# Kernel optimization log

Measured on AMD Instinct MI355X. Metric: run time of the kernel, lower is better.

The kernel has to match this reference:

```python
import jax, jax.numpy as jnp
import numpy as np
from jax import lax

EPS = 1e-5
K_UP = 5
RATIO = 2
PAD = 2


def conv1x1(x, w):
    # x: (B,C,H,W), w: (O,C)
    return jnp.einsum('bchw,oc->bohw', x, w)


def bn(x, g, b, m, v):
    inv = g / jnp.sqrt(v + EPS)
    return x * inv[None, :, None, None] + (b - m * inv)[None, :, None, None]


def relu6(x):
    return jnp.clip(x, 0.0, 6.0)


def carafe_down(x, wc, bc, we, be):
    # content-aware reassembly kernels
    y = conv1x1(x, wc) + bc[None, :, None, None]              # (B, 64, H, W)
    y = lax.conv_general_dilated(
        y, we, window_strides=(RATIO, RATIO), padding=[(PAD, PAD), (PAD, PAD)],
        dimension_numbers=('NCHW', 'OIHW', 'NCHW')) + be[None, :, None, None]
    w = jax.nn.softmax(y, axis=1)                              # (B, 25, Ho, Wo)
    B, C, H, W = x.shape
    Ho, Wo = H // RATIO, W // RATIO
    xp = jnp.pad(x, ((0, 0), (0, 0), (PAD, PAD), (PAD, PAD)))
    out = jnp.zeros((B, C, Ho, Wo), x.dtype)
    k = 0
    for i in range(K_UP):
        for j in range(K_UP):
            patch = xp[:, :, i:i + RATIO * Ho:RATIO, j:j + RATIO * Wo:RATIO]
            out = out + patch * w[:, k][:, None]
            k += 1
    return out


def setup_inputs() -> dict:
    key = jax.random.key(0)
    ks = jax.random.split(key, 20)
    B, INP, H, W = 8, 64, 112, 112
    OUP, HID, CMID = 128, 384, 64

    def bn_params(k, c):
        k1, k2, k3, k4 = jax.random.split(k, 4)
        return (jax.random.uniform(k1, (c,), jnp.float32, 0.5, 1.5),
                jax.random.normal(k2, (c,), jnp.float32) * 0.1,
                jax.random.normal(k3, (c,), jnp.float32) * 0.1,
                jax.random.uniform(k4, (c,), jnp.float32, 0.5, 1.5))
    g1, b1, m1, v1 = bn_params(ks[1], HID)
    g2, b2, m2, v2 = bn_params(ks[2], HID)
    g3, b3, m3, v3 = bn_params(ks[3], OUP)
    return {
        'x': jax.random.normal(ks[0], (B, INP, H, W), jnp.float32),
        'w1': jax.random.normal(ks[4], (HID, INP), jnp.float32) / np.sqrt(INP),
        'g1': g1, 'b1': b1, 'm1': m1, 'v1': v1,
        'wc': jax.random.normal(ks[5], (CMID, HID), jnp.float32) / np.sqrt(HID),
        'bc': jax.random.normal(ks[6], (CMID,), jnp.float32) * 0.01,
        'we': jax.random.normal(ks[7], (K_UP**2, CMID, 5, 5), jnp.float32) / np.sqrt(CMID * 25),
        'be': jax.random.normal(ks[8], (K_UP**2,), jnp.float32) * 0.01,
        'g2': g2, 'b2': b2, 'm2': m2, 'v2': v2,
        'w2': jax.random.normal(ks[9], (OUP, HID), jnp.float32) / np.sqrt(HID),
        'g3': g3, 'b3': b3, 'm3': m3, 'v3': v3,
    }


def reference(x, w1, g1, b1, m1, v1, wc, bc, we, be, g2, b2, m2, v2, w2, g3, b3, m3, v3):
    # stride-2 InvertedResidualBlockCarafe (no identity): 1x1 expand -> BN -> ReLU6
    # -> CARAFE_downsample -> BN -> ReLU6 -> 1x1 project -> BN
    h = relu6(bn(conv1x1(x, w1), g1, b1, m1, v1))
    h = relu6(bn(carafe_down(h, wc, bc, we, be), g2, b2, m2, v2))
    return bn(conv1x1(h, w2), g3, b3, m3, v3)
```

## Files before the change

### kernel.cpp

```cpp
#include <hip/hip_runtime.h>
#include <hip/hip_bf16.h>
#include <type_traits>

#define EPS 1e-5f

typedef _Float16 half8 __attribute__((ext_vector_type(8)));
typedef _Float16 half4 __attribute__((ext_vector_type(4)));
typedef _Float16 half2v __attribute__((ext_vector_type(2)));
typedef float f32x4 __attribute__((ext_vector_type(4)));

__device__ __forceinline__ void gload_lds16(const void* gsrc, void* ldst) {
  __builtin_amdgcn_global_load_lds(
      (const __attribute__((address_space(1))) void*)gsrc,
      (__attribute__((address_space(3))) void*)ldst, 16, 0, 0);
}

__global__ __launch_bounds__(256) void fold_k(
    const float* __restrict__ w1, const float* __restrict__ g1, const float* __restrict__ b1,
    const float* __restrict__ m1, const float* __restrict__ v1,
    const float* __restrict__ wc,
    const float* __restrict__ g2, const float* __restrict__ b2,
    const float* __restrict__ m2, const float* __restrict__ v2,
    const float* __restrict__ w2, const float* __restrict__ g3, const float* __restrict__ b3,
    const float* __restrict__ m3, const float* __restrict__ v3,
    const float* __restrict__ we,
    _Float16* __restrict__ w1h, float* __restrict__ bias1,
    _Float16* __restrict__ wch,
    _Float16* __restrict__ w2h, float* __restrict__ bias3,
    float* __restrict__ s2, float* __restrict__ t2,
    _Float16* __restrict__ wa) {
  int i = blockIdx.x * 256 + threadIdx.x;
  if (i < 384 * 64) {
    int o = i >> 6;
    float inv = g1[o] / sqrtf(v1[o] + EPS);
    w1h[i] = (_Float16)(w1[i] * inv);
  }
  if (i < 64 * 384) wch[i] = (_Float16)wc[i];
  if (i < 128 * 384) {
    int o = i / 384;
    float inv = g3[o] / sqrtf(v3[o] + EPS);
    w2h[i] = (_Float16)(w2[i] * inv);
  }
  if (i < 384) {
    float inv = g1[i] / sqrtf(v1[i] + EPS);
    bias1[i] = b1[i] - m1[i] * inv;
    float inv2 = g2[i] / sqrtf(v2[i] + EPS);
    s2[i] = inv2;
    t2[i] = b2[i] - m2[i] * inv2;
  }
  if (i < 128) {
    float inv = g3[i] / sqrtf(v3[i] + EPS);
    bias3[i] = b3[i] - m3[i] * inv;
  }
  if (i < 51200) {
    int j = i & 7;
    int lane = (i >> 3) & 63;
    int f = i >> 9;
    int ocf = f & 1;
    int tap = (f >> 1) % 25;
    int ph = f / 50;
    int oc = ocf * 16 + (lane & 15);
    int cm = ph * 32 + (lane >> 4) * 8 + j;
    float v = (oc < 25) ? we[((size_t)oc * 64 + cm) * 25 + tap] : 0.f;
    wa[i] = (_Float16)v;
  }
}

template <int IC, int NPF, int ACT, int NOC, int NPXT, typename TI, typename TO>
__global__ __launch_bounds__(256) void gemm16_k(
    const TI* __restrict__ in, const _Float16* __restrict__ wh,
    const float* __restrict__ bias, TO* __restrict__ out, int npx) {
  constexpr int BPX = NPF * 64;
  constexpr int V = 16 / sizeof(TI);
  constexpr int CPR = BPX / V;
  constexpr int SPT = 32 * CPR / 256;
  constexpr int PAD = 16 / sizeof(TO);
  constexpr int CH = 16 / sizeof(TO);
  constexpr int SPAN = NPF * 16;
  constexpr int LPO = SPAN / CH;
  constexpr int OCPI = 64 / LPO;
  constexpr size_t XS_B = (size_t)32 * BPX * sizeof(TI);
  constexpr size_t OT_B = (size_t)64 * (BPX + PAD) * sizeof(TO);
  constexpr size_t SM_B = XS_B > OT_B ? XS_B : OT_B;
  using vec16 = std::conditional_t<std::is_same_v<TO, _Float16>, half8, float4>;

  __shared__ __align__(16) unsigned char smem[SM_B];
  TI (*xs)[BPX] = (TI (*)[BPX])smem;
  TO (*oT)[BPX + PAD] = (TO (*)[BPX + PAD])smem;

  const int tid = threadIdx.x;
  const int lane = tid & 63;
  const int w = tid >> 6;
  const int l15 = lane & 15;
  const int g = lane >> 4;
  const int wpx = w * SPAN;

  const int wg = blockIdx.x;
  const int xcd = wg & 7;
  const int s = wg >> 3;
  const int oct = s % NOC;
  const int gl = s / NOC;
  const int grp = gl * 8 + xcd;
  const int pxt = grp % NPXT;
  const int b = grp / NPXT;

  const int p0 = pxt * BPX;
  const int oc0 = oct * 64;
  const int OCT = NOC * 64;
  const TI* inb = in + (size_t)b * IC * npx + p0;

  f32x4 acc[4][NPF];
#pragma unroll
  for (int fo = 0; fo < 4; ++fo)
#pragma unroll
    for (int pf = 0; pf < NPF; ++pf)
      acc[fo][pf] = (f32x4){0.f, 0.f, 0.f, 0.f};

  for (int kk = 0; kk < IC; kk += 32) {
    __syncthreads();
    half8 a[4];
#pragma unroll
    for (int fo = 0; fo < 4; ++fo)
      a[fo] = *(const half8*)&wh[(size_t)(oc0 + fo * 16 + l15) * IC + kk + g * 8];
#pragma unroll
    for (int i = 0; i < SPT; ++i) {
      int sl = tid + 256 * i;
      int k = sl / CPR, q = sl - (sl / CPR) * CPR;
      int qg = q ^ (((k >> 3) & 1) << 2);
      gload_lds16(&inb[(size_t)(kk + k) * npx + qg * V],
                  (unsigned char*)smem + (size_t)sl * 16);
    }
    __syncthreads();
    half8 xb[NPF];
#pragma unroll
    for (int pf = 0; pf < NPF; ++pf) {
      const int px = wpx + pf * 16 + l15;
      const int q = px / V, e = px - (px / V) * V;
      const int col = (q ^ ((g & 1) << 2)) * V + e;
#pragma unroll
      for (int j = 0; j < 8; ++j)
        xb[pf][j] = (_Float16)xs[g * 8 + j][col];
    }
#pragma unroll
    for (int fo = 0; fo < 4; ++fo)
#pragma unroll
      for (int pf = 0; pf < NPF; ++pf)
        acc[fo][pf] = __builtin_amdgcn_mfma_f32_16x16x32_f16(
            a[fo], xb[pf], acc[fo][pf], 0, 0, 0);
  }
  __syncthreads();

#pragma unroll
  for (int fo = 0; fo < 4; ++fo) {
#pragma unroll
    for (int r = 0; r < 4; ++r) {
      float bz = bias[oc0 + fo * 16 + g * 4 + r];
#pragma unroll
      for (int pf = 0; pf < NPF; ++pf) {
        float v = acc[fo][pf][r] + bz;
        if (ACT) v = fminf(fmaxf(v, 0.f), 6.f);
        oT[fo * 16 + g * 4 + r][wpx + pf * 16 + l15] = (TO)v;
      }
    }
  }
#pragma unroll
  for (int i = 0; i < LPO; ++i) {
    int oc = i * OCPI + lane / LPO;
    int pxo = (lane % LPO) * CH;
    vec16 v = *(const vec16*)&oT[oc][wpx + pxo];
    *(vec16*)&out[((size_t)b * OCT + oc0 + oc) * npx + p0 + wpx + pxo] = v;
  }
}

__global__ __launch_bounds__(256) void mask_conv6_k(
    const _Float16* __restrict__ y, const _Float16* __restrict__ wa,
    const float* __restrict__ be, float* __restrict__ msk) {
  __shared__ _Float16 ysh[32][5][136];
  __shared__ float lsm[32][66];
  const int ho = blockIdx.x;
  const int b = blockIdx.y;
  const int tid = threadIdx.x;
  const int lane = tid & 63;
  const int w = tid >> 6;
  const int l15 = lane & 15;
  const int g = lane >> 4;
  const int wo = w * 16 + l15;
  const int woe = (wo < 56) ? wo : 55;
  const int ci0 = 2 * woe + 6;

  for (int i = tid; i < 640; i += 256) {
    int ch = i / 20; int rem = i - ch * 20; int ri = rem / 4; int q = rem & 3;
    *(uint*)&ysh[ch][ri][q * 2] = 0u;
  }
  for (int i = tid; i < 1280; i += 256) {
    int ch = i / 40; int rem = i - ch * 40; int ri = rem / 8; int q = rem & 7;
    *(uint*)&ysh[ch][ri][120 + q * 2] = 0u;
  }

  f32x4 acc[2] = {(f32x4){0.f, 0.f, 0.f, 0.f}, (f32x4){0.f, 0.f, 0.f, 0.f}};

  for (int ph = 0; ph < 2; ++ph) {
    __syncthreads();
    for (int i = tid; i < 2240; i += 256) {
      int ch = i / 70;
      int rem = i - ch * 70;
      int ri = rem / 14;
      int j8 = rem - ri * 14;
      int hi = 2 * ho - 2 + ri;
      half8 v = {0, 0, 0, 0, 0, 0, 0, 0};
      if ((unsigned)hi < 112u)
        v = *(const half8*)&y[((size_t)(b * 64 + ph * 32 + ch) * 112 + hi) * 112 + j8 * 8];
      *(half8*)&ysh[ch][ri][8 + j8 * 8] = v;
    }
    __syncthreads();

    const _Float16* wap = wa + (size_t)ph * 25600;
#pragma unroll
    for (int di = 0; di < 5; ++di) {
      half2v pa[8], pb[8];
      _Float16 pc[8];
#pragma unroll
      for (int j = 0; j < 8; ++j) {
        pa[j] = *(const half2v*)&ysh[g * 8 + j][di][ci0];
        pb[j] = *(const half2v*)&ysh[g * 8 + j][di][ci0 + 2];
        pc[j] = ysh[g * 8 + j][di][ci0 + 4];
      }
#pragma unroll
      for (int dj = 0; dj < 5; ++dj) {
        half8 bf;
#pragma unroll
        for (int j = 0; j < 8; ++j)
          bf[j] = (dj == 0) ? pa[j][0]
                : (dj == 1) ? pa[j][1]
                : (dj == 2) ? pb[j][0]
                : (dj == 3) ? pb[j][1]
                            : pc[j];
        const int tap = di * 5 + dj;
        half8 a0 = *(const half8*)&wap[(tap * 2 + 0) * 512 + lane * 8];
        half8 a1 = *(const half8*)&wap[(tap * 2 + 1) * 512 + lane * 8];
        acc[0] = __builtin_amdgcn_mfma_f32_16x16x32_f16(a0, bf, acc[0], 0, 0, 0);
        acc[1] = __builtin_amdgcn_mfma_f32_16x16x32_f16(a1, bf, acc[1], 0, 0, 0);
      }
    }
  }

#pragma unroll
  for (int ocf = 0; ocf < 2; ++ocf)
#pragma unroll
    for (int r = 0; r < 4; ++r)
      lsm[ocf * 16 + g * 4 + r][w * 16 + l15] = acc[ocf][r];
  __syncthreads();

  if (tid < 56) {
    float v[25];
    float mx = -1e30f;
#pragma unroll
    for (int k = 0; k < 25; ++k) {
      float s = lsm[k][tid] + be[k];
      v[k] = s;
      mx = fmaxf(mx, s);
    }
    float s = 0.f;
#pragma unroll
    for (int k = 0; k < 25; ++k) {
      v[k] = __expf(v[k] - mx);
      s += v[k];
    }
    float inv = 1.0f / s;
#pragma unroll
    for (int k = 0; k < 25; ++k)
      msk[((size_t)b * 25 + k) * 3136 + ho * 56 + tid] = v[k] * inv;
  }
}

__device__ __forceinline__ void stage_pair(float dst[2][19][120],
                                           const _Float16* __restrict__ hbase,
                                           int ho0, int tid) {
  for (int i = tid; i < 2 * 19 * 14; i += 512) {
    int ch = i / 266;
    int rem = i - ch * 266;
    int rr = rem / 14;
    int j8 = rem - rr * 14;
    int hi = 2 * ho0 - 2 + rr;
    float4 lo = {0.f, 0.f, 0.f, 0.f}, hi4 = {0.f, 0.f, 0.f, 0.f};
    if ((unsigned)hi < 112u) {
      half8 v = *(const half8*)&hbase[(size_t)ch * 12544 + hi * 112 + j8 * 8];
      lo = (float4){(float)v[0], (float)v[1], (float)v[2], (float)v[3]};
      hi4 = (float4){(float)v[4], (float)v[5], (float)v[6], (float)v[7]};
    }
    *(float4*)&dst[ch][rr][4 + j8 * 8] = lo;
    *(float4*)&dst[ch][rr][8 + j8 * 8] = hi4;
  }
}

__global__ __launch_bounds__(512) void carafe3_k(
    const _Float16* __restrict__ h, const float* __restrict__ msk,
    const float* __restrict__ s2, const float* __restrict__ t2,
    _Float16* __restrict__ h2) {
  __shared__ float ys[2][2][19][120];
  const int hx = blockIdx.x;
  const int b  = blockIdx.y;
  const int cz = blockIdx.z;
  const int ho0 = hx * 8;
  const int tid = threadIdx.x;
  const int r = tid / 56;
  const int c = tid - r * 56;
  const int c0 = cz * 24;

  for (int i = tid; i < 2 * 2 * 19 * 8; i += 512) {
    int bufi = i / 304;
    int rem = i - bufi * 304;
    int ch = rem / 152;
    int rem2 = rem - ch * 152;
    int rr = rem2 / 8;
    int p = rem2 - rr * 8;
    int col = (p < 4) ? p : (112 + p);
    ys[bufi][ch][rr][col] = 0.f;
  }

  float m[25];
  if (tid < 448) {
    const float* mp = msk + (size_t)b * 25 * 3136 + (ho0 + r) * 56 + c;
#pragma unroll
    for (int k = 0; k < 25; ++k) m[k] = mp[(size_t)k * 3136];
  }
  __syncthreads();

  stage_pair(ys[0], h + (size_t)(b * 384 + c0) * 12544, ho0, tid);
  __syncthreads();

#pragma unroll
  for (int p = 0; p < 12; ++p) {
    const int bf = p & 1;
    if (p + 1 < 12)
      stage_pair(ys[bf ^ 1], h + (size_t)(b * 384 + c0 + 2 * (p + 1)) * 12544,
                 ho0, tid);
    if (tid < 448) {
#pragma unroll
      for (int cl = 0; cl < 2; ++cl) {
        const int cc = c0 + 2 * p + cl;
        float acc = 0.f;
#pragma unroll
        for (int di = 0; di < 5; ++di) {
          const float* row = &ys[bf][cl][2 * r + di][2 * c + 2];
          float2 a01 = *(const float2*)&row[0];
          float2 a23 = *(const float2*)&row[2];
          float a4 = row[4];
          acc = fmaf(a01.x, m[di * 5 + 0], acc);
          acc = fmaf(a01.y, m[di * 5 + 1], acc);
          acc = fmaf(a23.x, m[di * 5 + 2], acc);
          acc = fmaf(a23.y, m[di * 5 + 3], acc);
          acc = fmaf(a4,    m[di * 5 + 4], acc);
        }
        float o = s2[cc] * acc + t2[cc];
        h2[((size_t)(b * 384 + cc) * 56 + ho0 + r) * 56 + c] =
            (_Float16)fminf(fmaxf(o, 0.f), 6.f);
      }
    }
    __syncthreads();
  }
}

extern "C" void kernel_launch(void* const* d_in, const int* in_sizes, int n_in,
                              void* d_out, int out_size, void* d_ws, size_t ws_size,
                              hipStream_t stream) {
  const float* x  = (const float*)d_in[0];
  const float* w1 = (const float*)d_in[1];
  const float* g1 = (const float*)d_in[2];
  const float* b1 = (const float*)d_in[3];
  const float* m1 = (const float*)d_in[4];
  const float* v1 = (const float*)d_in[5];
  const float* wc = (const float*)d_in[6];
  const float* bc = (const float*)d_in[7];
  const float* we = (const float*)d_in[8];
  const float* be = (const float*)d_in[9];
  const float* g2 = (const float*)d_in[10];
  const float* b2 = (const float*)d_in[11];
  const float* m2 = (const float*)d_in[12];
  const float* v2 = (const float*)d_in[13];
  const float* w2 = (const float*)d_in[14];
  const float* g3 = (const float*)d_in[15];
  const float* b3 = (const float*)d_in[16];
  const float* m3 = (const float*)d_in[17];
  const float* v3 = (const float*)d_in[18];
  float* out = (float*)d_out;

  _Float16* hq  = (_Float16*)d_ws;
  _Float16* yq  = hq + 38535168;
  _Float16* h2q = yq + 6422528;
  float* mskf   = (float*)(h2q + 9633792);
  float* bias1  = mskf + 627200;
  float* bias3  = bias1 + 384;
  float* s2     = bias3 + 128;
  float* t2     = s2 + 384;
  _Float16* w1h = (_Float16*)(t2 + 384);
  _Float16* wch = w1h + 24576;
  _Float16* w2h = wch + 24576;
  _Float16* wa  = w2h + 49152;

  fold_k<<<200, 256, 0, stream>>>(w1, g1, b1, m1, v1, wc, g2, b2, m2, v2,
                                  w2, g3, b3, m3, v3, we,
                                  w1h, bias1, wch, w2h, bias3, s2, t2, wa);

  gemm16_k<64, 2, 1, 6, 98, float, _Float16>
      <<<6 * 98 * 8, 256, 0, stream>>>(x, w1h, bias1, hq, 12544);

  gemm16_k<384, 2, 0, 1, 98, _Float16, _Float16>
      <<<1 * 98 * 8, 256, 0, stream>>>(hq, wch, bc, yq, 12544);

  mask_conv6_k<<<dim3(56, 8), 256, 0, stream>>>(yq, wa, be, mskf);

  carafe3_k<<<dim3(7, 8, 16), 512, 0, stream>>>(hq, mskf, s2, t2, h2q);

  gemm16_k<384, 1, 0, 2, 49, _Float16, float>
      <<<2 * 49 * 8, 256, 0, stream>>>(h2q, w2h, bias3, out, 3136);
}
```

Measured before the change: 146.6 us.

## Fuse expand 1x1 conv with content-encoder 1x1 conv in one kernel

Replaces the two separate GEMM launches (expand conv + BN/ReLU6, then the 384->64 content conv) with one kernel that computes each 64-pixel tile of the hidden activations in LDS and immediately feeds it into the second MFMA GEMM. It still writes the hidden activations to global memory for the CARAFE gather, but avoids re-reading them for the second GEMM and saves a launch. The trade-off is smaller tiles (64 pixels per block), extra barriers per hidden chunk, and weights reloaded from global per block.

New measurement: 185.3 us. +26.5%, slower.

```diff
diff --git a/kernel.cpp b/kernel.cpp
--- a/kernel.cpp
+++ b/kernel.cpp
@@ -63,6 +63,111 @@
     int cm = ph * 32 + (lane >> 4) * 8 + j;
     float v = (oc < 25) ? we[((size_t)oc * 64 + cm) * 25 + tap] : 0.f;
     wa[i] = (_Float16)v;
+  }
+}
+
+__global__ __launch_bounds__(256) void fused2_k(
+    const float* __restrict__ x, const _Float16* __restrict__ w1h,
+    const float* __restrict__ bias1, const _Float16* __restrict__ wch,
+    const float* __restrict__ bc, _Float16* __restrict__ hq,
+    _Float16* __restrict__ yq) {
+  __shared__ __align__(16) float xh[64][64];
+  __shared__ _Float16 hT[64][76];
+
+  const int tid = threadIdx.x;
+  const int lane = tid & 63;
+  const int w = tid >> 6;
+  const int l15 = lane & 15;
+  const int g = lane >> 4;
+  const int wpx = w * 16;
+  const int p0 = blockIdx.x * 64;
+  const int b = blockIdx.y;
+  const float* inb = x + (size_t)b * 64 * 12544 + p0;
+
+#pragma unroll
+  for (int i = 0; i < 4; ++i) {
+    int sl = tid + 256 * i;
+    int k = sl >> 4, q = sl & 15;
+    int qg = q ^ (((k >> 3) & 1) << 2);
+    gload_lds16(&inb[(size_t)k * 12544 + qg * 4],
+                (unsigned char*)xh + (size_t)sl * 16);
+  }
+  __syncthreads();
+
+  half8 xb[2];
+  {
+    const int px = wpx + l15;
+    const int q = px >> 2, e = px & 3;
+    const int col = (q ^ ((g & 1) << 2)) * 4 + e;
+#pragma unroll
+    for (int ks = 0; ks < 2; ++ks)
+#pragma unroll
+      for (int j = 0; j < 8; ++j)
+        xb[ks][j] = (_Float16)xh[ks * 32 + g * 8 + j][col];
+  }
+
+  f32x4 acc2[4];
+#pragma unroll
+  for (int fo2 = 0; fo2 < 4; ++fo2) acc2[fo2] = (f32x4){0.f, 0.f, 0.f, 0.f};
+
+#pragma unroll
+  for (int t = 0; t < 6; ++t) {
+    f32x4 acc1[4];
+#pragma unroll
+    for (int fo = 0; fo < 4; ++fo) acc1[fo] = (f32x4){0.f, 0.f, 0.f, 0.f};
+#pragma unroll
+    for (int ks = 0; ks < 2; ++ks)
+#pragma unroll
+      for (int fo = 0; fo < 4; ++fo) {
+        half8 a = *(const half8*)&w1h[(size_t)(t * 64 + fo * 16 + l15) * 64 + ks * 32 + g * 8];
+        acc1[fo] = __builtin_amdgcn_mfma_f32_16x16x32_f16(a, xb[ks], acc1[fo], 0, 0, 0);
+      }
+    __syncthreads();
+#pragma unroll
+    for (int fo = 0; fo < 4; ++fo)
+#pragma unroll
+      for (int r = 0; r < 4; ++r) {
+        int ocl = fo * 16 + g * 4 + r;
+        float v = acc1[fo][r] + bias1[t * 64 + ocl];
+        v = fminf(fmaxf(v, 0.f), 6.f);
+        hT[ocl][wpx + l15] = (_Float16)v;
+      }
+    __syncthreads();
+#pragma unroll
+    for (int i = 0; i < 4; ++i) {
+      int sl = tid + 256 * i;
+      int row = sl >> 4, j4 = sl & 15;
+      half4 v = *(const half4*)&hT[row][j4 * 4];
+      *(half4*)&hq[(size_t)(b * 384 + t * 64 + row) * 12544 + p0 + j4 * 4] = v;
+    }
+#pragma unroll
+    for (int ks = 0; ks < 2; ++ks) {
+      half8 bf;
+#pragma unroll
+      for (int j = 0; j < 8; ++j) bf[j] = hT[ks * 32 + g * 8 + j][wpx + l15];
+#pragma unroll
+      for (int fo2 = 0; fo2 < 4; ++fo2) {
+        half8 a2 = *(const half8*)&wch[(size_t)(fo2 * 16 + l15) * 384 + t * 64 + ks * 32 + g * 8];
+        acc2[fo2] = __builtin_amdgcn_mfma_f32_16x16x32_f16(a2, bf, acc2[fo2], 0, 0, 0);
+      }
+    }
+  }
+  __syncthreads();
+
+#pragma unroll
+  for (int fo2 = 0; fo2 < 4; ++fo2)
+#pragma unroll
+    for (int r = 0; r < 4; ++r) {
+      int oc2 = fo2 * 16 + g * 4 + r;
+      hT[oc2][wpx + l15] = (_Float16)(acc2[fo2][r] + bc[oc2]);
+    }
+  __syncthreads();
+#pragma unroll
+  for (int i = 0; i < 4; ++i) {
+    int sl = tid + 256 * i;
+    int row = sl >> 4, j4 = sl & 15;
+    half4 v = *(const half4*)&hT[row][j4 * 4];
+    *(half4*)&yq[(size_t)(b * 64 + row) * 12544 + p0 + j4 * 4] = v;
   }
 }
 
@@ -402,11 +507,7 @@
                                   w2, g3, b3, m3, v3, we,
                                   w1h, bias1, wch, w2h, bias3, s2, t2, wa);
 
-  gemm16_k<64, 2, 1, 6, 98, float, _Float16>
-      <<<6 * 98 * 8, 256, 0, stream>>>(x, w1h, bias1, hq, 12544);
-
-  gemm16_k<384, 2, 0, 1, 98, _Float16, _Float16>
-      <<<1 * 98 * 8, 256, 0, stream>>>(hq, wch, bc, yq, 12544);
+  fused2_k<<<dim3(196, 8), 256, 0, stream>>>(x, w1h, bias1, wch, bc, hq, yq);
 
   mask_conv6_k<<<dim3(56, 8), 256, 0, stream>>>(yq, wa, be, mskf);
 
```
